# Optimization experiments

Hardware: AMD Instinct MI355X
Metric: run time of the kernel (lower is better)

Reference implementation:

```python
import jax, jax.numpy as jnp
import numpy as np

N_PIX = 100000
N_LINES = 3000
WL_LO, WL_HI = 9000.0, 11000.0


def setup_inputs() -> dict:
    key = jax.random.key(0)
    k1, k2, k3, k4 = jax.random.split(key, 4)
    wl = jnp.linspace(WL_LO, WL_HI, N_PIX, dtype=jnp.float32)
    # line centers inside the wavelength span (sorted for realism)
    lam_centers = jnp.sort(
        jax.random.uniform(k1, (N_LINES,), jnp.float32, WL_LO + 30.0, WL_HI - 30.0)
    )
    # log-amplitudes: exp(.) ~ 0.01 - 0.1 so prod(1 - a*V) stays positive
    amplitudes = jnp.log(jax.random.uniform(k2, (N_LINES,), jnp.float32, 0.01, 0.1))
    # log-widths: exp(.) ~ 0.05 - 0.5 Angstrom
    sigma_widths = jnp.log(jax.random.uniform(k3, (N_LINES,), jnp.float32, 0.05, 0.5))
    gamma_widths = jnp.log(jax.random.uniform(k4, (N_LINES,), jnp.float32, 0.05, 0.5))
    return {
        "wl": wl,
        "lam_centers": lam_centers,
        "amplitudes": amplitudes,
        "sigma_widths": sigma_widths,
        "gamma_widths": gamma_widths,
        "a_coeff": jnp.float32(1.0),
        "b_coeff": jnp.float32(0.0),
        "c_coeff": jnp.float32(0.0),
    }


def _pseudo_voigt(wl, lam_centers, amplitudes, sigma_widths, gamma_widths):
    """(n_lines, n_pix) pseudo-Voigt profile matrix, faithful to the torch math."""
    sigma = jnp.exp(sigma_widths)[:, None]  # (L,1)
    gamma = jnp.exp(gamma_widths)[:, None]  # (L,1)
    fwhm_G = 2.3548 * sigma
    fwhm_L = 2.0 * gamma
    fwhm = (
        fwhm_G**5
        + 2.69269 * fwhm_G**4 * fwhm_L
        + 2.42843 * fwhm_G**3 * fwhm_L**2
        + 4.47163 * fwhm_G**2 * fwhm_L**3
        + 0.07842 * fwhm_G * fwhm_L**4
        + fwhm_L**5
    ) ** (1.0 / 5.0)
    f_ratio = fwhm_L / fwhm
    eta = 1.36603 * f_ratio - 0.47719 * f_ratio**2 + 0.11116 * f_ratio**3
    d = wl[None, :] - lam_centers[:, None]  # (L,P)
    lorentz = (1.0 / 3.141592654) * gamma / (gamma**2 + d**2)
    gauss = 1.0 / (sigma * 2.5066) * jnp.exp(-0.5 * (d / sigma) ** 2)
    return jnp.exp(amplitudes)[:, None] * (eta * lorentz + (1.0 - eta) * gauss)


def reference(wl, lam_centers, amplitudes, sigma_widths, gamma_widths,
              a_coeff, b_coeff, c_coeff):
    wl_normed = (wl - 10500.0) / 2500.0
    poly = a_coeff + b_coeff * wl_normed + c_coeff * wl_normed**2
    V = _pseudo_voigt(wl, lam_centers, amplitudes, sigma_widths, gamma_widths)
    return jnp.prod(1.0 - V, axis=0) * poly
```

## Files before the change

### kernel.cpp

```cpp
#include <hip/hip_runtime.h>
#include <math.h>


#define PX      64
#define D_LOR   10.0f
#define D_GAU   3.5f
#define TILE    64

__device__ __forceinline__ int lower_bound_f(const float* __restrict__ a,
                                             int n, float v) {
    int lo = 0, len = n;
    while (len > 0) {
        int half = len >> 1;
        int mid = lo + half;
        if (a[mid] < v) { lo = mid + 1; len -= half + 1; }
        else            { len = half; }
    }
    return lo;
}

__global__ void __launch_bounds__(PX) fused_voigt_kernel(
        const float* __restrict__ wl,
        const float* __restrict__ lam,
        const float* __restrict__ amp_log,
        const float* __restrict__ sig_log,
        const float* __restrict__ gam_log,
        const float* __restrict__ a_c,
        const float* __restrict__ b_c,
        const float* __restrict__ c_c,
        float* __restrict__ out,
        int n_pix, int n_lines) {
    __shared__ float4 q_s[TILE];
    __shared__ float  ag_s[TILE];

    const int tid = threadIdx.x;
    const int p   = blockIdx.x * PX + tid;
    const int pc  = min(p, n_pix - 1);
    const float w = wl[pc];

    const float w0 = __shfl(w, 0);
    const float w1 = __shfl(w, PX - 1);
    const int lo = lower_bound_f(lam, n_lines, w0 - D_LOR);
    const int hi = lower_bound_f(lam, n_lines, w1 + D_LOR);

    float prod0 = 1.0f, prod1 = 1.0f, prod2 = 1.0f, prod3 = 1.0f;

    for (int t = lo; t < hi; t += TILE) {
        const int nt = min(TILE, hi - t);
        __syncthreads();
        if (tid < nt) {
            const int l = t + tid;
            float sigma = __expf(sig_log[l]);
            float gamma = __expf(gam_log[l]);
            float amp   = __expf(amp_log[l]);
            float fG = 2.3548f * sigma;
            float fL = 2.0f * gamma;
            float fG2 = fG * fG, fL2 = fL * fL;
            float fwhm5 = fG2 * fG2 * fG
                        + 2.69269f * fG2 * fG2 * fL
                        + 2.42843f * fG2 * fG  * fL2
                        + 4.47163f * fG2 * fL2 * fL
                        + 0.07842f * fG  * fL2 * fL2
                        + fL2 * fL2 * fL;
            float fwhm = __expf(0.2f * __logf(fwhm5));
            float fr   = fL * __builtin_amdgcn_rcpf(fwhm);
            float eta  = fr * (1.36603f + fr * (-0.47719f + fr * 0.11116f));
            float Al   = amp * eta * gamma * (1.0f / 3.141592654f);
            float Ag   = amp * (1.0f - eta) *
                         __builtin_amdgcn_rcpf(sigma * 2.5066f);
            q_s[tid]  = make_float4(lam[l], Al, gamma * gamma,
                                    -0.5f / (sigma * sigma));
            ag_s[tid] = Ag;
        }
        __syncthreads();

        int i = 0;
        for (; i + 3 < nt; i += 4) {
            float4 qa = q_s[i];
            float4 qb = q_s[i + 1];
            float4 qc = q_s[i + 2];
            float4 qd = q_s[i + 3];
            float da = w - qa.x, db = w - qb.x, dc = w - qc.x, dd = w - qd.x;
            float da2 = da * da, db2 = db * db, dc2 = dc * dc, dd2 = dd * dd;
            float va = qa.y * __builtin_amdgcn_rcpf(qa.z + da2);
            float vb = qb.y * __builtin_amdgcn_rcpf(qb.z + db2);
            float vc = qc.y * __builtin_amdgcn_rcpf(qc.z + dc2);
            float vd = qd.y * __builtin_amdgcn_rcpf(qd.z + dd2);
            if (fabsf(da) < D_GAU) va += ag_s[i]     * __expf(qa.w * da2);
            if (fabsf(db) < D_GAU) vb += ag_s[i + 1] * __expf(qb.w * db2);
            if (fabsf(dc) < D_GAU) vc += ag_s[i + 2] * __expf(qc.w * dc2);
            if (fabsf(dd) < D_GAU) vd += ag_s[i + 3] * __expf(qd.w * dd2);
            prod0 *= (1.0f - va);
            prod1 *= (1.0f - vb);
            prod2 *= (1.0f - vc);
            prod3 *= (1.0f - vd);
        }
        for (; i < nt; ++i) {
            float4 q = q_s[i];
            float d  = w - q.x;
            float d2 = d * d;
            float v  = q.y * __builtin_amdgcn_rcpf(q.z + d2);
            if (fabsf(d) < D_GAU) v += ag_s[i] * __expf(q.w * d2);
            prod0 *= (1.0f - v);
        }
    }

    if (p < n_pix) {
        float wn = (w - 10500.0f) * (1.0f / 2500.0f);
        float poly = a_c[0] + wn * (b_c[0] + wn * c_c[0]);
        out[p] = (prod0 * prod1) * (prod2 * prod3) * poly;
    }
}

extern "C" void kernel_launch(void* const* d_in, const int* in_sizes, int n_in,
                              void* d_out, int out_size, void* d_ws, size_t ws_size,
                              hipStream_t stream) {
    const float* wl      = (const float*)d_in[0];
    const float* lam     = (const float*)d_in[1];
    const float* amp_log = (const float*)d_in[2];
    const float* sig_log = (const float*)d_in[3];
    const float* gam_log = (const float*)d_in[4];
    const float* a_c     = (const float*)d_in[5];
    const float* b_c     = (const float*)d_in[6];
    const float* c_c     = (const float*)d_in[7];
    float* out = (float*)d_out;

    int n_pix   = in_sizes[0];
    int n_lines = in_sizes[1];
    int n_blocks = (n_pix + PX - 1) / PX;

    fused_voigt_kernel<<<n_blocks, PX, 0, stream>>>(
        wl, lam, amp_log, sig_log, gam_log, a_c, b_c, c_c, out,
        n_pix, n_lines);
}
```

Measured before the change: 74.87 us.

## Split line loop across four wavefronts per pixel block and reduce partial products

Each block now uses four wavefronts that cover the same 64 pixels, each handling an interleaved subset of the lines in the tile; partial products are combined through shared memory at the end. The two binary searches for the line window now run in parallel on two lanes of wave 0 and are shared via LDS. This is meant to cut per-wave serial latency and raise occupancy for a grid of only about 1.5k small blocks, at the cost of an extra barrier and a shared-memory reduction. Only 64 threads compute line parameters per tile, so the other waves wait at the barrier during that step.

```diff
diff --git a/kernel.cpp b/kernel.cpp
--- a/kernel.cpp
+++ b/kernel.cpp
@@ -2,10 +2,12 @@
 #include <math.h>
 
 
-#define PX      64
-#define D_LOR   10.0f
-#define D_GAU   3.5f
-#define TILE    64
+#define PX       64
+#define NW       4
+#define NTHREADS (PX * NW)
+#define D_LOR    10.0f
+#define D_GAU    3.5f
+#define TILE     64
 
 __device__ __forceinline__ int lower_bound_f(const float* __restrict__ a,
                                              int n, float v) {
@@ -19,7 +21,7 @@
     return lo;
 }
 
-__global__ void __launch_bounds__(PX) fused_voigt_kernel(
+__global__ void __launch_bounds__(NTHREADS) fused_voigt_kernel(
         const float* __restrict__ wl,
         const float* __restrict__ lam,
         const float* __restrict__ amp_log,
@@ -32,18 +34,32 @@
         int n_pix, int n_lines) {
     __shared__ float4 q_s[TILE];
     __shared__ float  ag_s[TILE];
+    __shared__ float  part[NW][PX];
+    __shared__ int    bnd[2];
 
-    const int tid = threadIdx.x;
-    const int p   = blockIdx.x * PX + tid;
-    const int pc  = min(p, n_pix - 1);
-    const float w = wl[pc];
+    const int tid  = threadIdx.x;
+    const int wv   = tid >> 6;
+    const int lane = tid & 63;
+    const int p    = blockIdx.x * PX + lane;
+    const int pc   = min(p, n_pix - 1);
+    const float w  = wl[pc];
 
-    const float w0 = __shfl(w, 0);
-    const float w1 = __shfl(w, PX - 1);
-    const int lo = lower_bound_f(lam, n_lines, w0 - D_LOR);
-    const int hi = lower_bound_f(lam, n_lines, w1 + D_LOR);
+    const float ac = a_c[0];
+    const float bc = b_c[0];
+    const float cc = c_c[0];
 
-    float prod0 = 1.0f, prod1 = 1.0f, prod2 = 1.0f, prod3 = 1.0f;
+    if (wv == 0) {
+        const float w0 = __shfl(w, 0)      - D_LOR;
+        const float w1 = __shfl(w, PX - 1) + D_LOR;
+        const float v  = (lane & 1) ? w1 : w0;
+        const int r = lower_bound_f(lam, n_lines, v);
+        if (lane < 2) bnd[lane] = r;
+    }
+    __syncthreads();
+    const int lo = bnd[0];
+    const int hi = bnd[1];
+
+    float prod0 = 1.0f, prod1 = 1.0f;
 
     for (int t = lo; t < hi; t += TILE) {
         const int nt = min(TILE, hi - t);
@@ -74,28 +90,20 @@
         }
         __syncthreads();
 
-        int i = 0;
-        for (; i + 3 < nt; i += 4) {
+        int i = wv;
+        for (; i + NW < nt; i += 2 * NW) {
             float4 qa = q_s[i];
-            float4 qb = q_s[i + 1];
-            float4 qc = q_s[i + 2];
-            float4 qd = q_s[i + 3];
-            float da = w - qa.x, db = w - qb.x, dc = w - qc.x, dd = w - qd.x;
-            float da2 = da * da, db2 = db * db, dc2 = dc * dc, dd2 = dd * dd;
+            float4 qb = q_s[i + NW];
+            float da = w - qa.x, db = w - qb.x;
+            float da2 = da * da, db2 = db * db;
             float va = qa.y * __builtin_amdgcn_rcpf(qa.z + da2);
             float vb = qb.y * __builtin_amdgcn_rcpf(qb.z + db2);
-            float vc = qc.y * __builtin_amdgcn_rcpf(qc.z + dc2);
-            float vd = qd.y * __builtin_amdgcn_rcpf(qd.z + dd2);
-            if (fabsf(da) < D_GAU) va += ag_s[i]     * __expf(qa.w * da2);
-            if (fabsf(db) < D_GAU) vb += ag_s[i + 1] * __expf(qb.w * db2);
-            if (fabsf(dc) < D_GAU) vc += ag_s[i + 2] * __expf(qc.w * dc2);
-            if (fabsf(dd) < D_GAU) vd += ag_s[i + 3] * __expf(qd.w * dd2);
+            if (fabsf(da) < D_GAU) va += ag_s[i]      * __expf(qa.w * da2);
+            if (fabsf(db) < D_GAU) vb += ag_s[i + NW] * __expf(qb.w * db2);
             prod0 *= (1.0f - va);
             prod1 *= (1.0f - vb);
-            prod2 *= (1.0f - vc);
-            prod3 *= (1.0f - vd);
         }
-        for (; i < nt; ++i) {
+        for (; i < nt; i += NW) {
             float4 q = q_s[i];
             float d  = w - q.x;
             float d2 = d * d;
@@ -105,10 +113,14 @@
         }
     }
 
-    if (p < n_pix) {
+    part[wv][lane] = prod0 * prod1;
+    __syncthreads();
+
+    if (wv == 0 && p < n_pix) {
         float wn = (w - 10500.0f) * (1.0f / 2500.0f);
-        float poly = a_c[0] + wn * (b_c[0] + wn * c_c[0]);
-        out[p] = (prod0 * prod1) * (prod2 * prod3) * poly;
+        float poly = ac + wn * (bc + wn * cc);
+        out[p] = (part[0][lane] * part[1][lane]) *
+                 (part[2][lane] * part[3][lane]) * poly;
     }
 }
 
@@ -129,7 +141,7 @@
     int n_lines = in_sizes[1];
     int n_blocks = (n_pix + PX - 1) / PX;
 
-    fused_voigt_kernel<<<n_blocks, PX, 0, stream>>>(
+    fused_voigt_kernel<<<n_blocks, NTHREADS, 0, stream>>>(
         wl, lam, amp_log, sig_log, gam_log, a_c, b_c, c_c, out,
         n_pix, n_lines);
 }
```

Result: faster. 71.40 us (-4.6%).
